# Kernel optimization log

Measured on AMD Instinct MI355X. Metric: run time of the kernel, lower is better.

Reference implementation:

```python
import jax, jax.numpy as jnp
import numpy as np

N_NODES = 50000


def gcn_conv(h, W, b, src, dst, n_nodes):
    # PyG GCNConv: h' = D^{-1/2} (A + I) D^{-1/2} (h @ W) + b
    h = h @ W  # [N, out]
    deg = jax.ops.segment_sum(jnp.ones_like(dst, dtype=h.dtype), dst, num_segments=n_nodes)
    dinv = jnp.where(deg > 0, jax.lax.rsqrt(deg), 0.0)  # [N]
    norm = dinv[src] * dinv[dst]  # [E]
    msg = h[src] * norm[:, None]  # [E, out]
    out = jax.ops.segment_sum(msg, dst, num_segments=n_nodes)
    return out + b


def setup_inputs() -> dict:
    key = jax.random.key(0)
    ks = jax.random.split(key, 12)
    N, E, P, D, H = N_NODES, 1600000, 200000, 128, 128
    s = lambda fan_in: 1.0 / np.sqrt(fan_in)
    return {
        "x": jax.random.normal(ks[0], (N, D), dtype=jnp.float32),
        "edge_index": jax.random.randint(ks[1], (2, E), 0, N, dtype=jnp.int32),
        "drug_pairs": jax.random.randint(ks[2], (P, 2), 0, N, dtype=jnp.int32),
        "W1": jax.random.normal(ks[3], (D, H), dtype=jnp.float32) * s(D),
        "b1": jnp.zeros((H,), dtype=jnp.float32),
        "W2": jax.random.normal(ks[4], (H, H), dtype=jnp.float32) * s(H),
        "b2": jnp.zeros((H,), dtype=jnp.float32),
        "Wh1": jax.random.normal(ks[5], (2 * H, H), dtype=jnp.float32) * s(2 * H),
        "bh1": jnp.zeros((H,), dtype=jnp.float32),
        "Wh2": jax.random.normal(ks[6], (H, 1), dtype=jnp.float32) * s(H),
        "bh2": jnp.zeros((1,), dtype=jnp.float32),
    }


def reference(x, edge_index, drug_pairs, W1, b1, W2, b2, Wh1, bh1, Wh2, bh2):
    n = x.shape[0]
    # add self-loops once (GCNConv default add_self_loops=True)
    loop = jnp.arange(n, dtype=edge_index.dtype)
    src = jnp.concatenate([edge_index[0], loop])
    dst = jnp.concatenate([edge_index[1], loop])

    h = jax.nn.relu(gcn_conv(x, W1, b1, src, dst, n))  # dropout = identity (eval)
    h = jax.nn.relu(gcn_conv(h, W2, b2, src, dst, n))

    combined = jnp.concatenate([h[drug_pairs[:, 0]], h[drug_pairs[:, 1]]], axis=1)  # [P, 2H]
    out = jax.nn.relu(combined @ Wh1 + bh1) @ Wh2 + bh2  # [P, 1]
    return out
```

## Files before the change

### kernel.cpp

```cpp
#include <hip/hip_runtime.h>
#include <hip/hip_fp16.h>


#define BSH 9
#define BSZ (1 << BSH)
#define MSB 4096

typedef __attribute__((ext_vector_type(8))) short bf16x8;
typedef __attribute__((ext_vector_type(4))) float f32x4;

__global__ __launch_bounds__(256) void k_zero_i32(int* __restrict__ p, int n) {
  int i = blockIdx.x * 256 + threadIdx.x;
  if (i < n) p[i] = 0;
}

__global__ __launch_bounds__(256) void k_bucket_hist(const int* __restrict__ dst,
                                                     int* __restrict__ gcnt,
                                                     int e, int kb) {
  __shared__ int h[128];
  int tid = threadIdx.x;
  if (tid < kb) h[tid] = 0;
  __syncthreads();
  int stride = gridDim.x * 256;
  for (int i = blockIdx.x * 256 + tid; i < e; i += stride) {
    int d = __builtin_nontemporal_load(&dst[i]);
    atomicAdd(&h[d >> BSH], 1);
  }
  __syncthreads();
  if (tid < kb) atomicAdd(&gcnt[tid], h[tid]);
}

__global__ __launch_bounds__(128) void k_bucket_scan(const int* __restrict__ gcnt,
                                                     int* __restrict__ gbase,
                                                     int* __restrict__ gcur,
                                                     int kb) {
  __shared__ int ws[2];
  int t = threadIdx.x;
  int lane = t & 63, w = t >> 6;
  int v = (t < kb) ? gcnt[t] : 0;
  int orig = v;
#pragma unroll
  for (int o = 1; o < 64; o <<= 1) {
    int u = __shfl_up(v, o, 64);
    if (lane >= o) v += u;
  }
  if (lane == 63) ws[w] = v;
  __syncthreads();
  int ex = ((w == 1) ? ws[0] : 0) + v - orig;
  if (t < kb) { gbase[t] = ex; gcur[t] = ex; }
  if (t == kb - 1) gbase[kb] = ex + orig;
}

__global__ __launch_bounds__(256) void k_multisplit(const int* __restrict__ src,
                                                    const int* __restrict__ dst,
                                                    int* __restrict__ gcur,
                                                    int* __restrict__ tmp,
                                                    int e, int kb) {
  __shared__ int h[128], base[128];
  int tid = threadIdx.x;
  if (tid < kb) h[tid] = 0;
  __syncthreads();
  int i0 = blockIdx.x * MSB + tid;
  int d[16], rk[16];
#pragma unroll
  for (int u = 0; u < 16; ++u) {
    int i = i0 + u * 256;
    if (i < e) {
      d[u] = __builtin_nontemporal_load(&dst[i]);
      rk[u] = atomicAdd(&h[d[u] >> BSH], 1);
    }
  }
  __syncthreads();
  if (tid < kb && h[tid] > 0) base[tid] = atomicAdd(&gcur[tid], h[tid]);
  __syncthreads();
#pragma unroll
  for (int u = 0; u < 16; ++u) {
    int i = i0 + u * 256;
    if (i < e) {
      int s = __builtin_nontemporal_load(&src[i]);
      tmp[base[d[u] >> BSH] + rk[u]] = ((d[u] & (BSZ - 1)) << 16) | s;
    }
  }
}

__global__ __launch_bounds__(512) void k_bucket_build(
    const int* __restrict__ tmp, const int* __restrict__ gbase,
    int* __restrict__ rowptr, float* __restrict__ dinv,
    int* __restrict__ colarr, int n, int kb, int e) {
  __shared__ int dl[BSZ], cl[BSZ], ws[8];
  int t = threadIdx.x, b = blockIdx.x;
  int s0 = gbase[b], s1 = gbase[b + 1];
  dl[t] = 0;
  __syncthreads();
  for (int j = s0 + t; j < s1; j += 512)
    atomicAdd(&dl[((unsigned)tmp[j]) >> 16], 1);
  __syncthreads();
  int lane = t & 63, w = t >> 6;
  int v = dl[t], orig = v;
#pragma unroll
  for (int o = 1; o < 64; o <<= 1) {
    int u = __shfl_up(v, o, 64);
    if (lane >= o) v += u;
  }
  if (lane == 63) ws[w] = v;
  __syncthreads();
  if (t == 0) {
    int a = 0;
#pragma unroll
    for (int k = 0; k < 8; ++k) { int x = ws[k]; ws[k] = a; a += x; }
  }
  __syncthreads();
  int ex = ws[w] + v - orig;
  cl[t] = ex;
  int node = (b << BSH) + t;
  if (node < n) {
    rowptr[node] = s0 + ex;
    dinv[node] = rsqrtf((float)(orig + 1));
  }
  if (b == kb - 1 && t == 0) rowptr[n] = e;
  __syncthreads();
  for (int j = s0 + t; j < s1; j += 512) {
    int p = tmp[j];
    int r = atomicAdd(&cl[((unsigned)p) >> 16], 1);
    colarr[s0 + r] = p & 0xFFFF;
  }
}

__device__ __forceinline__ void split8(const float* v, bf16x8& hi, bf16x8& lo) {
#pragma unroll
  for (int j = 0; j < 8; ++j) {
    unsigned u = __float_as_uint(v[j]);
    hi[j] = (short)(u >> 16);
    float lf = v[j] - __uint_as_float(u & 0xffff0000u);
    lo[j] = (short)(__float_as_uint(lf) >> 16);
  }
}

__global__ __launch_bounds__(256) void k_prep_w(
    const float* __restrict__ W1, const float* __restrict__ W2,
    const float* __restrict__ Wh1, short* __restrict__ fragH,
    short* __restrict__ fragL) {
  int g = blockIdx.x * 256 + threadIdx.x;
  if (g >= 4 * 2048) return;
  int w = g >> 11;
  int rem = g & 2047;
  int lane = rem & 63;
  int ts = rem >> 6;
  int t = ts >> 2, s = ts & 3;
  int n = (t << 4) + (lane & 15);
  int k0 = s * 32 + (lane >> 4) * 8;
  const float* W = (w == 0) ? W1 : (w == 1) ? W2 : (w == 2) ? Wh1 : (Wh1 + 128 * 128);
  short h[8], l[8];
#pragma unroll
  for (int j = 0; j < 8; ++j) {
    float x = W[(k0 + j) * 128 + n];
    unsigned u = __float_as_uint(x);
    h[j] = (short)(u >> 16);
    float lf = x - __uint_as_float(u & 0xffff0000u);
    l[j] = (short)(__float_as_uint(lf) >> 16);
  }
  ((int4*)fragH)[g] = *(int4*)h;
  ((int4*)fragL)[g] = *(int4*)l;
}

__global__ __launch_bounds__(256) void k_gemm_mfma(
    const float* __restrict__ X, const short* __restrict__ fragH,
    const short* __restrict__ fragL, const float* __restrict__ rowscale,
    __half* __restrict__ C16, int n) {
  int wid = threadIdx.x >> 6, lane = threadIdx.x & 63;
  int r0 = (blockIdx.x * 4 + wid) * 16;
  if (r0 >= n) return;
  int m = lane & 15, quad = lane >> 4;
  const float* xrow = X + (size_t)(r0 + m) * 128;
  f32x4 acc[8];
#pragma unroll
  for (int t = 0; t < 8; ++t) acc[t] = (f32x4)(0.f);
  const int4* FH = (const int4*)fragH;
  const int4* FL = (const int4*)fragL;
#pragma unroll
  for (int s = 0; s < 4; ++s) {
    int k0 = s * 32 + quad * 8;
    float xv[8];
    *(float4*)&xv[0] = *(const float4*)(xrow + k0);
    *(float4*)&xv[4] = *(const float4*)(xrow + k0 + 4);
    bf16x8 ah, al;
    split8(xv, ah, al);
#pragma unroll
    for (int t = 0; t < 8; ++t) {
      int idx = (t * 4 + s) * 64 + lane;
      bf16x8 bh = *(const bf16x8*)&FH[idx];
      bf16x8 bl = *(const bf16x8*)&FL[idx];
      acc[t] = __builtin_amdgcn_mfma_f32_16x16x32_bf16(ah, bh, acc[t], 0, 0, 0);
      acc[t] = __builtin_amdgcn_mfma_f32_16x16x32_bf16(al, bh, acc[t], 0, 0, 0);
      acc[t] = __builtin_amdgcn_mfma_f32_16x16x32_bf16(ah, bl, acc[t], 0, 0, 0);
    }
  }
  float sc[4];
#pragma unroll
  for (int r = 0; r < 4; ++r)
    sc[r] = rowscale ? rowscale[r0 + quad * 4 + r] : 1.f;
#pragma unroll
  for (int t = 0; t < 8; ++t) {
#pragma unroll
    for (int r = 0; r < 4; ++r) {
      int row = r0 + quad * 4 + r;
      C16[(size_t)row * 128 + t * 16 + m] = __float2half(acc[t][r] * sc[r]);
    }
  }
}

__global__ __launch_bounds__(256) void k_agg_h(
    const __half2* __restrict__ g2, const float* __restrict__ dinv,
    const int* __restrict__ rowptr, const int* __restrict__ col,
    const float* __restrict__ bias, float* __restrict__ out, int n) {
  int i = blockIdx.x * 4 + (threadIdx.x >> 6);
  int c = threadIdx.x & 63;
  if (i >= n) return;
  float2 a0 = __half22float2(g2[(size_t)i * 64 + c]);
  float2 a1 = make_float2(0.f, 0.f);
  float2 a2 = make_float2(0.f, 0.f);
  float2 a3 = make_float2(0.f, 0.f);
  int beg = rowptr[i], end = rowptr[i + 1];
  int j = beg;
  for (; j + 4 <= end; j += 4) {
    int s0 = __builtin_nontemporal_load(&col[j]);
    int s1 = __builtin_nontemporal_load(&col[j + 1]);
    int s2 = __builtin_nontemporal_load(&col[j + 2]);
    int s3 = __builtin_nontemporal_load(&col[j + 3]);
    float2 v0 = __half22float2(g2[(size_t)s0 * 64 + c]);
    float2 v1 = __half22float2(g2[(size_t)s1 * 64 + c]);
    float2 v2 = __half22float2(g2[(size_t)s2 * 64 + c]);
    float2 v3 = __half22float2(g2[(size_t)s3 * 64 + c]);
    a0.x += v0.x; a0.y += v0.y;
    a1.x += v1.x; a1.y += v1.y;
    a2.x += v2.x; a2.y += v2.y;
    a3.x += v3.x; a3.y += v3.y;
  }
  for (; j < end; ++j) {
    float2 v = __half22float2(g2[(size_t)__builtin_nontemporal_load(&col[j]) * 64 + c]);
    a0.x += v.x; a0.y += v.y;
  }
  float di = dinv[i];
  float2 bi = ((const float2*)bias)[c];
  float2 o;
  o.x = fmaxf(fmaf(di, (a0.x + a1.x) + (a2.x + a3.x), bi.x), 0.f);
  o.y = fmaxf(fmaf(di, (a0.y + a1.y) + (a2.y + a3.y), bi.y), 0.f);
  ((float2*)out)[(size_t)i * 64 + c] = o;
}

__global__ __launch_bounds__(256) void k_pairs_h(
    const __half2* __restrict__ A, const __half2* __restrict__ B,
    const int* __restrict__ pairs, const float* __restrict__ bh1,
    const float* __restrict__ wh2, const float* __restrict__ bh2,
    float* __restrict__ out, int P) {
  int p = blockIdx.x * 4 + (threadIdx.x >> 6);
  int c = threadIdx.x & 63;
  if (p >= P) return;
  int p0 = pairs[2 * p], p1 = pairs[2 * p + 1];
  float2 av = __half22float2(A[(size_t)p0 * 64 + c]);
  float2 bv = __half22float2(B[(size_t)p1 * 64 + c]);
  float2 bi = ((const float2*)bh1)[c];
  float2 wv = ((const float2*)wh2)[c];
  float v0 = fmaxf(av.x + bv.x + bi.x, 0.f) * wv.x;
  float v1 = fmaxf(av.y + bv.y + bi.y, 0.f) * wv.y;
  float s = v0 + v1;
#pragma unroll
  for (int o = 32; o > 0; o >>= 1) s += __shfl_down(s, o, 64);
  if (c == 0) out[p] = s + bh2[0];
}

extern "C" void kernel_launch(void* const* d_in, const int* in_sizes, int n_in,
                              void* d_out, int out_size, void* d_ws, size_t ws_size,
                              hipStream_t stream) {
  const float* x   = (const float*)d_in[0];
  const int* ei    = (const int*)d_in[1];
  const int* pairs = (const int*)d_in[2];
  const float* W1  = (const float*)d_in[3];
  const float* b1  = (const float*)d_in[4];
  const float* W2  = (const float*)d_in[5];
  const float* b2  = (const float*)d_in[6];
  const float* Wh1 = (const float*)d_in[7];
  const float* bh1 = (const float*)d_in[8];
  const float* Wh2 = (const float*)d_in[9];
  const float* bh2 = (const float*)d_in[10];
  (void)n_in; (void)out_size; (void)ws_size;

  int N = in_sizes[0] / 128;
  int E = in_sizes[1] / 2;
  int P = in_sizes[2] / 2;
  const int* src = ei;
  const int* dst = ei + E;
  int KB = (N + BSZ - 1) >> BSH;

  char* wsp = (char*)d_ws;
  size_t off = 0;
  auto alloc = [&](size_t bytes) -> void* {
    void* p = wsp + off;
    off += (bytes + 255) & ~(size_t)255;
    return p;
  };
  __half* g16 = (__half*)alloc((size_t)N * 128 * 2);
  float* h1   = (float*)alloc((size_t)N * 128 * 4);
  float* h2   = (float*)alloc((size_t)N * 128 * 4);
  float* dinv = (float*)alloc((size_t)N * 4);
  int* rowptr = (int*)alloc((size_t)(N + 1) * 4);
  int* colarr = (int*)alloc((size_t)E * 4);
  int* tmp    = (int*)alloc((size_t)E * 4);
  short* fragH = (short*)alloc(4 * 2048 * 8 * 2);
  short* fragL = (short*)alloc(4 * 2048 * 8 * 2);
  int* gcnt  = (int*)alloc((size_t)(KB + 1) * 4);
  int* gbase = (int*)alloc((size_t)(KB + 1) * 4);
  int* gcur  = (int*)alloc((size_t)(KB + 1) * 4);
  __half* A16 = g16;
  __half* B16 = (__half*)h1;
  short* fH_W1 = fragH + 0 * 16384;  short* fL_W1 = fragL + 0 * 16384;
  short* fH_W2 = fragH + 1 * 16384;  short* fL_W2 = fragL + 1 * 16384;
  short* fH_Wa = fragH + 2 * 16384;  short* fL_Wa = fragL + 2 * 16384;
  short* fH_Wb = fragH + 3 * 16384;  short* fL_Wb = fragL + 3 * 16384;

  k_prep_w<<<32, 256, 0, stream>>>(W1, W2, Wh1, fragH, fragL);

  k_zero_i32<<<1, 256, 0, stream>>>(gcnt, KB + 1);
  k_bucket_hist<<<256, 256, 0, stream>>>(dst, gcnt, E, KB);
  k_bucket_scan<<<1, 128, 0, stream>>>(gcnt, gbase, gcur, KB);
  k_multisplit<<<(E + MSB - 1) / MSB, 256, 0, stream>>>(src, dst, gcur, tmp, E, KB);
  k_bucket_build<<<KB, 512, 0, stream>>>(tmp, gbase, rowptr, dinv, colarr, N, KB, E);

  int GB = (N / 16 + 3) / 4;
  int AB = (N + 3) / 4;
  k_gemm_mfma<<<GB, 256, 0, stream>>>(x, fH_W1, fL_W1, dinv, g16, N);
  k_agg_h<<<AB, 256, 0, stream>>>((const __half2*)g16, dinv, rowptr, colarr, b1, h1, N);
  k_gemm_mfma<<<GB, 256, 0, stream>>>(h1, fH_W2, fL_W2, dinv, g16, N);
  k_agg_h<<<AB, 256, 0, stream>>>((const __half2*)g16, dinv, rowptr, colarr, b2, h2, N);
  k_gemm_mfma<<<GB, 256, 0, stream>>>(h2, fH_Wa, fL_Wa, nullptr, A16, N);
  k_gemm_mfma<<<GB, 256, 0, stream>>>(h2, fH_Wb, fL_Wb, nullptr, B16, N);
  k_pairs_h<<<(P + 3) / 4, 256, 0, stream>>>((const __half2*)A16, (const __half2*)B16,
                                             pairs, bh1, Wh2, bh2, (float*)d_out, P);
}
```

Before: 413.6 us.

## Split aggregation into column slices with edge-parallel lanes and shuffle reduction

The CSR aggregation kernel now gives each node to four blocks, one per 16-column slice. Within a wavefront, four lane groups each process a different neighbor edge at once, and their partial sums are combined with cross-lane shuffles. This exposes more concurrent gathers per wave and shortens the serial edge loop per lane. In exchange, each neighbor row is read as four 64-byte segments spread across blocks, and the rowptr/col reads are repeated four times.

```diff
diff --git a/kernel.cpp b/kernel.cpp
--- a/kernel.cpp
+++ b/kernel.cpp
@@ -209,43 +209,47 @@
   }
 }
 
-__global__ __launch_bounds__(256) void k_agg_h(
+__global__ __launch_bounds__(256) void k_agg_s(
     const __half2* __restrict__ g2, const float* __restrict__ dinv,
     const int* __restrict__ rowptr, const int* __restrict__ col,
     const float* __restrict__ bias, float* __restrict__ out, int n) {
-  int i = blockIdx.x * 4 + (threadIdx.x >> 6);
-  int c = threadIdx.x & 63;
+  int sl = blockIdx.x & 3;
+  int rb = blockIdx.x >> 2;
+  int wid = threadIdx.x >> 6, lane = threadIdx.x & 63;
+  int i = rb * 4 + wid;
   if (i >= n) return;
-  float2 a0 = __half22float2(g2[(size_t)i * 64 + c]);
-  float2 a1 = make_float2(0.f, 0.f);
-  float2 a2 = make_float2(0.f, 0.f);
-  float2 a3 = make_float2(0.f, 0.f);
+  int e = lane >> 4;
+  int c = sl * 16 + (lane & 15);
   int beg = rowptr[i], end = rowptr[i + 1];
+  float2 a0 = make_float2(0.f, 0.f), a1 = make_float2(0.f, 0.f);
+  if (e == 0) a0 = __half22float2(g2[(size_t)i * 64 + c]);
   int j = beg;
-  for (; j + 4 <= end; j += 4) {
-    int s0 = __builtin_nontemporal_load(&col[j]);
-    int s1 = __builtin_nontemporal_load(&col[j + 1]);
-    int s2 = __builtin_nontemporal_load(&col[j + 2]);
-    int s3 = __builtin_nontemporal_load(&col[j + 3]);
+  for (; j + 8 <= end; j += 8) {
+    int s0 = __builtin_nontemporal_load(&col[j + e]);
+    int s1 = __builtin_nontemporal_load(&col[j + 4 + e]);
     float2 v0 = __half22float2(g2[(size_t)s0 * 64 + c]);
     float2 v1 = __half22float2(g2[(size_t)s1 * 64 + c]);
-    float2 v2 = __half22float2(g2[(size_t)s2 * 64 + c]);
-    float2 v3 = __half22float2(g2[(size_t)s3 * 64 + c]);
     a0.x += v0.x; a0.y += v0.y;
     a1.x += v1.x; a1.y += v1.y;
-    a2.x += v2.x; a2.y += v2.y;
-    a3.x += v3.x; a3.y += v3.y;
-  }
-  for (; j < end; ++j) {
-    float2 v = __half22float2(g2[(size_t)__builtin_nontemporal_load(&col[j]) * 64 + c]);
-    a0.x += v.x; a0.y += v.y;
-  }
-  float di = dinv[i];
-  float2 bi = ((const float2*)bias)[c];
-  float2 o;
-  o.x = fmaxf(fmaf(di, (a0.x + a1.x) + (a2.x + a3.x), bi.x), 0.f);
-  o.y = fmaxf(fmaf(di, (a0.y + a1.y) + (a2.y + a3.y), bi.y), 0.f);
-  ((float2*)out)[(size_t)i * 64 + c] = o;
+  }
+  for (; j < end; j += 4) {
+    if (j + e < end) {
+      int s0 = __builtin_nontemporal_load(&col[j + e]);
+      float2 v0 = __half22float2(g2[(size_t)s0 * 64 + c]);
+      a0.x += v0.x; a0.y += v0.y;
+    }
+  }
+  float sx = a0.x + a1.x, sy = a0.y + a1.y;
+  sx += __shfl_down(sx, 32, 64); sx += __shfl_down(sx, 16, 64);
+  sy += __shfl_down(sy, 32, 64); sy += __shfl_down(sy, 16, 64);
+  if (e == 0) {
+    float di = dinv[i];
+    float2 bi = ((const float2*)bias)[c];
+    float2 o;
+    o.x = fmaxf(fmaf(di, sx, bi.x), 0.f);
+    o.y = fmaxf(fmaf(di, sy, bi.y), 0.f);
+    ((float2*)out)[(size_t)i * 64 + c] = o;
+  }
 }
 
 __global__ __launch_bounds__(256) void k_pairs_h(
@@ -327,11 +331,11 @@
   k_bucket_build<<<KB, 512, 0, stream>>>(tmp, gbase, rowptr, dinv, colarr, N, KB, E);
 
   int GB = (N / 16 + 3) / 4;
-  int AB = (N + 3) / 4;
+  int AGB = ((N + 3) / 4) * 4;
   k_gemm_mfma<<<GB, 256, 0, stream>>>(x, fH_W1, fL_W1, dinv, g16, N);
-  k_agg_h<<<AB, 256, 0, stream>>>((const __half2*)g16, dinv, rowptr, colarr, b1, h1, N);
+  k_agg_s<<<AGB, 256, 0, stream>>>((const __half2*)g16, dinv, rowptr, colarr, b1, h1, N);
   k_gemm_mfma<<<GB, 256, 0, stream>>>(h1, fH_W2, fL_W2, dinv, g16, N);
-  k_agg_h<<<AB, 256, 0, stream>>>((const __half2*)g16, dinv, rowptr, colarr, b2, h2, N);
+  k_agg_s<<<AGB, 256, 0, stream>>>((const __half2*)g16, dinv, rowptr, colarr, b2, h2, N);
   k_gemm_mfma<<<GB, 256, 0, stream>>>(h2, fH_Wa, fL_Wa, nullptr, A16, N);
   k_gemm_mfma<<<GB, 256, 0, stream>>>(h2, fH_Wb, fL_Wb, nullptr, B16, N);
   k_pairs_h<<<(P + 3) / 4, 256, 0, stream>>>((const __half2*)A16, (const __half2*)B16,
```

Result: slower. 566.2 us (+36.9%).

## Store CSR column indices as 16-bit and stage GEMM input rows through LDS

Applied to the files above, without the earlier changes.

The CSR column array becomes unsigned short instead of int. This halves the index traffic read by both aggregation passes and written by the bucket build, and relies on node ids fitting in 16 bits, which the packed temporary format already assumed. The MFMA GEMM now loads a 64-row tile of X into padded shared memory with coalesced float2 loads before the per-wave fragment reads. The cost is LDS use and a block-wide barrier per GEMM block.

```diff
diff --git a/kernel.cpp b/kernel.cpp
--- a/kernel.cpp
+++ b/kernel.cpp
@@ -5,6 +5,7 @@
 #define BSH 9
 #define BSZ (1 << BSH)
 #define MSB 4096
+#define XPAD 132
 
 typedef __attribute__((ext_vector_type(8))) short bf16x8;
 typedef __attribute__((ext_vector_type(4))) float f32x4;
@@ -86,7 +87,7 @@
 __global__ __launch_bounds__(512) void k_bucket_build(
     const int* __restrict__ tmp, const int* __restrict__ gbase,
     int* __restrict__ rowptr, float* __restrict__ dinv,
-    int* __restrict__ colarr, int n, int kb, int e) {
+    unsigned short* __restrict__ colarr, int n, int kb, int e) {
   __shared__ int dl[BSZ], cl[BSZ], ws[8];
   int t = threadIdx.x, b = blockIdx.x;
   int s0 = gbase[b], s1 = gbase[b + 1];
@@ -122,7 +123,7 @@
   for (int j = s0 + t; j < s1; j += 512) {
     int p = tmp[j];
     int r = atomicAdd(&cl[((unsigned)p) >> 16], 1);
-    colarr[s0 + r] = p & 0xFFFF;
+    colarr[s0 + r] = (unsigned short)(p & 0xFFFF);
   }
 }
 
@@ -167,11 +168,24 @@
     const float* __restrict__ X, const short* __restrict__ fragH,
     const short* __restrict__ fragL, const float* __restrict__ rowscale,
     __half* __restrict__ C16, int n) {
-  int wid = threadIdx.x >> 6, lane = threadIdx.x & 63;
-  int r0 = (blockIdx.x * 4 + wid) * 16;
+  __shared__ float sX[64 * XPAD];
+  int tid = threadIdx.x;
+  int row0 = blockIdx.x * 64;
+  const float2* X2 = (const float2*)(X + (size_t)row0 * 128);
+#pragma unroll
+  for (int it = 0; it < 16; ++it) {
+    int t = it * 256 + tid;
+    int r = t >> 6, c2 = t & 63;
+    int gr = row0 + r;
+    float2 v = (gr < n) ? X2[t] : make_float2(0.f, 0.f);
+    *(float2*)&sX[r * XPAD + c2 * 2] = v;
+  }
+  __syncthreads();
+  int wid = tid >> 6, lane = tid & 63;
+  int r0 = row0 + wid * 16;
   if (r0 >= n) return;
   int m = lane & 15, quad = lane >> 4;
-  const float* xrow = X + (size_t)(r0 + m) * 128;
+  const float* xrow = sX + (wid * 16 + m) * XPAD;
   f32x4 acc[8];
 #pragma unroll
   for (int t = 0; t < 8; ++t) acc[t] = (f32x4)(0.f);
@@ -181,8 +195,10 @@
   for (int s = 0; s < 4; ++s) {
     int k0 = s * 32 + quad * 8;
     float xv[8];
-    *(float4*)&xv[0] = *(const float4*)(xrow + k0);
-    *(float4*)&xv[4] = *(const float4*)(xrow + k0 + 4);
+    *(float2*)&xv[0] = *(const float2*)(xrow + k0);
+    *(float2*)&xv[2] = *(const float2*)(xrow + k0 + 2);
+    *(float2*)&xv[4] = *(const float2*)(xrow + k0 + 4);
+    *(float2*)&xv[6] = *(const float2*)(xrow + k0 + 6);
     bf16x8 ah, al;
     split8(xv, ah, al);
 #pragma unroll
@@ -211,7 +227,7 @@
 
 __global__ __launch_bounds__(256) void k_agg_h(
     const __half2* __restrict__ g2, const float* __restrict__ dinv,
-    const int* __restrict__ rowptr, const int* __restrict__ col,
+    const int* __restrict__ rowptr, const unsigned short* __restrict__ col,
     const float* __restrict__ bias, float* __restrict__ out, int n) {
   int i = blockIdx.x * 4 + (threadIdx.x >> 6);
   int c = threadIdx.x & 63;
@@ -237,7 +253,8 @@
     a3.x += v3.x; a3.y += v3.y;
   }
   for (; j < end; ++j) {
-    float2 v = __half22float2(g2[(size_t)__builtin_nontemporal_load(&col[j]) * 64 + c]);
+    int s0 = __builtin_nontemporal_load(&col[j]);
+    float2 v = __half22float2(g2[(size_t)s0 * 64 + c]);
     a0.x += v.x; a0.y += v.y;
   }
   float di = dinv[i];
@@ -304,7 +321,7 @@
   float* h2   = (float*)alloc((size_t)N * 128 * 4);
   float* dinv = (float*)alloc((size_t)N * 4);
   int* rowptr = (int*)alloc((size_t)(N + 1) * 4);
-  int* colarr = (int*)alloc((size_t)E * 4);
+  unsigned short* colarr = (unsigned short*)alloc((size_t)E * 2);
   int* tmp    = (int*)alloc((size_t)E * 4);
   short* fragH = (short*)alloc(4 * 2048 * 8 * 2);
   short* fragL = (short*)alloc(4 * 2048 * 8 * 2);
@@ -326,7 +343,7 @@
   k_multisplit<<<(E + MSB - 1) / MSB, 256, 0, stream>>>(src, dst, gcur, tmp, E, KB);
   k_bucket_build<<<KB, 512, 0, stream>>>(tmp, gbase, rowptr, dinv, colarr, N, KB, E);
 
-  int GB = (N / 16 + 3) / 4;
+  int GB = (N + 63) / 64;
   int AB = (N + 3) / 4;
   k_gemm_mfma<<<GB, 256, 0, stream>>>(x, fH_W1, fL_W1, dinv, g16, N);
   k_agg_h<<<AB, 256, 0, stream>>>((const __half2*)g16, dinv, rowptr, colarr, b1, h1, N);
```

Result: faster. 404.5 us (-2.2%).
